# Performance work log

Measured on AMD Instinct MI355X. Metric: run time of the kernel, lower is better.

The kernel has to match this reference:

```python
import jax, jax.numpy as jnp
import numpy as np

N_E = 8192
DIM = 256
BETA = 0.25


def _l2norm(x, eps=1e-12):
    # matches F.normalize(p=2, dim=-1): x / max(||x||, eps)
    n = jnp.sqrt(jnp.sum(x * x, axis=-1, keepdims=True))
    return x / jnp.maximum(n, eps)


def setup_inputs() -> dict:
    key = jax.random.key(0)
    k1, k2 = jax.random.split(key)
    z = jax.random.normal(k1, (8, 1024, DIM), dtype=jnp.float32)
    embedding_weight = jax.random.normal(k2, (N_E, DIM), dtype=jnp.float32)
    return {"z": z, "embedding_weight": embedding_weight}


def reference(z, embedding_weight):
    z = _l2norm(z)                                   # [B,S,D]
    zf = z.reshape(-1, DIM)                          # [N,D]
    embed_norm = _l2norm(embedding_weight)           # [n_e,D]
    # d = ||z||^2 + ||e||^2 - 2 z.e  -> [N, n_e]
    d = (jnp.sum(zf * zf, axis=1, keepdims=True)
         + jnp.sum(embed_norm * embed_norm, axis=1)
         - 2.0 * jnp.einsum('bd,nd->bn', zf, embed_norm))
    encoding_indices = jnp.argmin(d, axis=1).reshape(z.shape[:-1])  # [B,S]
    z_q = embedding_weight[encoding_indices]          # gather raw codes
    z_q = _l2norm(z_q)                                # [B,S,D]
    loss = (BETA * jnp.mean((jax.lax.stop_gradient(z_q) - z) ** 2)
            + jnp.mean((z_q - jax.lax.stop_gradient(z)) ** 2))
    z_q = z + jax.lax.stop_gradient(z_q - z)          # straight-through
    return z_q, loss, encoding_indices
```

## Files before the change

kernel.cpp:

```cpp
#include <hip/hip_runtime.h>
#include <hip/hip_fp16.h>
#include <cfloat>
#include <math.h>

#define DIM    256
#define N_TOK  8192
#define N_E    8192
#define NSEG   1024
#define MARGIN 0.012f

typedef __attribute__((ext_vector_type(8))) short bf16x8;
typedef __attribute__((ext_vector_type(4))) float f32x4;
typedef __attribute__((ext_vector_type(8))) unsigned short ushort8;

__device__ __forceinline__ unsigned short f2bf(float f) {
    unsigned u = __float_as_uint(f);
    unsigned r = u + 0x7fff + ((u >> 16) & 1);
    return (unsigned short)(r >> 16);
}
__device__ __forceinline__ unsigned fkey(float f) {
    unsigned u = __float_as_uint(f);
    return (u & 0x80000000u) ? ~u : (u | 0x80000000u);
}
__device__ __forceinline__ unsigned short f2h(float f) {
    const __half h = __float2half(f);
    return *(const unsigned short*)&h;
}
__device__ __forceinline__ float h2f(unsigned short u) {
    __half_raw r; r.x = u;
    return __half2float((__half)r);
}

__global__ __launch_bounds__(256) void l2norm_all(const float* __restrict__ z,
                                                  const float* __restrict__ emb,
                                                  float* __restrict__ zn,
                                                  unsigned short* __restrict__ zb,
                                                  float* __restrict__ en,
                                                  unsigned short* __restrict__ esw,
                                                  float* __restrict__ e2) {
    const int lane = threadIdx.x & 63;
    const bool isE = blockIdx.x < (N_E / 4);
    const int row = (isE ? blockIdx.x : blockIdx.x - N_E / 4) * 4 + (threadIdx.x >> 6);
    const float* in = isE ? emb : z;
    float* out = isE ? en : zn;
    const float4 v = *(const float4*)(in + row * DIM + lane * 4);
    float s = v.x * v.x + v.y * v.y + v.z * v.z + v.w * v.w;
#pragma unroll
    for (int off = 1; off < 64; off <<= 1) s += __shfl_xor(s, off, 64);
    const float inv = 1.0f / fmaxf(sqrtf(s), 1e-12f);
    const float4 o = make_float4(v.x * inv, v.y * inv, v.z * inv, v.w * inv);
    *(float4*)(out + row * DIM + lane * 4) = o;
    ushort4 ob; ob.x = f2bf(o.x); ob.y = f2bf(o.y); ob.z = f2bf(o.z); ob.w = f2bf(o.w);
    const int k0 = lane * 4;
    if (isE) {
        const size_t sidx = ((size_t)((row >> 4) * 8 + (k0 >> 5)) * 64
                             + ((k0 >> 3) & 3) * 16 + (row & 15)) * 8 + (k0 & 7);
        *(ushort4*)(esw + sidx) = ob;
        float q = o.x * o.x + o.y * o.y + o.z * o.z + o.w * o.w;
#pragma unroll
        for (int off = 1; off < 64; off <<= 1) q += __shfl_xor(q, off, 64);
        if (lane == 0) e2[row] = q;
    } else {
        *(ushort4*)(zb + (size_t)row * DIM + k0) = ob;
    }
}

__global__ __launch_bounds__(256, 3) void mfma_dist(const unsigned short* __restrict__ zb,
                                                    const unsigned short* __restrict__ esw,
                                                    unsigned short* __restrict__ segMh) {
    __shared__ __align__(16) unsigned short As[2][128 * 64];
    float* sm = reinterpret_cast<float*>(As);

    const int tid  = threadIdx.x;
    const int lane = tid & 63;
    const int wave = tid >> 6;
    const int wm = wave & 1, wn = wave >> 1;
    const int row0 = (blockIdx.x & 63) * 128;
    const int col0 = (blockIdx.x >> 6) * 128;
    const int fr = lane & 15, q = lane >> 4;

    f32x4 acc[4][4];
#pragma unroll
    for (int ci = 0; ci < 4; ci++)
#pragma unroll
        for (int zi = 0; zi < 4; zi++) acc[ci][zi] = (f32x4){0.f, 0.f, 0.f, 0.f};

    const int aBase = (col0 >> 4) + wn * 4;
    auto la = [&](int i, int kc) {
        return *(const bf16x8*)(esw + (size_t)(aBase + i) * 4096 + kc * 512 + lane * 8);
    };
    const int cxor = (lane & 7) ^ ((lane >> 3) & 7);
    const unsigned short* gZ = zb + (size_t)(row0 + wave * 32 + (lane >> 3)) * DIM + cxor * 8;
    auto stage = [&](int buf, int p) {
#pragma unroll
        for (int j = 0; j < 4; j++) {
            __builtin_amdgcn_global_load_lds(
                (const __attribute__((address_space(1))) unsigned int*)(gZ + (size_t)j * 8 * DIM + p * 64),
                (__attribute__((address_space(3))) unsigned int*)&As[buf][(wave * 32 + j * 8) * 64],
                16, 0, 0);
        }
    };
    auto lz = [&](int buf, int i, int h) {
        const int r = wm * 64 + i * 16 + fr;
        const int slot = (h * 4 + q) ^ (fr & 7);
        return *(const bf16x8*)&As[buf][r * 64 + slot * 8];
    };

    bf16x8 ca[8][4];
    stage(0, 0);
    __builtin_amdgcn_sched_barrier(0);
#pragma unroll
    for (int kc = 0; kc < 2; kc++)
#pragma unroll
        for (int i = 0; i < 4; i++) ca[kc][i] = la(i, kc);

#pragma unroll
    for (int p = 0; p < 4; p++) {
        asm volatile("s_waitcnt vmcnt(8)" ::: "memory");
        __builtin_amdgcn_s_barrier();
        __builtin_amdgcn_sched_barrier(0);
        if (p < 3) {
            stage((p + 1) & 1, p + 1);
            __builtin_amdgcn_sched_barrier(0);
        }
#pragma unroll
        for (int h = 0; h < 2; h++) {
            const int kc = 2 * p + h;
            if (kc + 2 < 8) {
#pragma unroll
                for (int i = 0; i < 4; i++) ca[kc + 2][i] = la(i, kc + 2);
            }
            bf16x8 zfr[4];
#pragma unroll
            for (int i = 0; i < 4; i++) zfr[i] = lz(p & 1, i, h);
#pragma unroll
            for (int ci = 0; ci < 4; ci++)
#pragma unroll
                for (int zi = 0; zi < 4; zi++)
                    acc[ci][zi] = __builtin_amdgcn_mfma_f32_16x16x32_bf16(ca[kc][ci], zfr[zi], acc[ci][zi], 0, 0, 0);
        }
    }

#pragma unroll
    for (int ci = 0; ci < 4; ci++) {
#pragma unroll
        for (int zi = 0; zi < 4; zi++) {
            const float t0 = fmaf(-2.0f, acc[ci][zi][0], 1.0f);
            const float t1 = fmaf(-2.0f, acc[ci][zi][1], 1.0f);
            const float t2 = fmaf(-2.0f, acc[ci][zi][2], 1.0f);
            const float t3 = fmaf(-2.0f, acc[ci][zi][3], 1.0f);
            float mm = fminf(fminf(t0, t1), fminf(t2, t3));
            mm = fminf(mm, __shfl_xor(mm, 16, 64));
            if (q == 0) sm[wave * 512 + (ci * 2 + 0) * 64 + zi * 16 + fr] = mm;
            if (q == 2) sm[wave * 512 + (ci * 2 + 1) * 64 + zi * 16 + fr] = mm;
        }
    }
    ushort8 o8;
#pragma unroll
    for (int j = 0; j < 8; j++) o8[j] = f2h(sm[wave * 512 + j * 64 + lane]);
    *(ushort8*)&segMh[(size_t)(row0 + wm * 64 + lane) * NSEG + (col0 >> 3) + wn * 8] = o8;
}

__global__ __launch_bounds__(256) void select_rescore(const unsigned short* __restrict__ segMh,
                                                      const float* __restrict__ en,
                                                      const float* __restrict__ e2,
                                                      float* zq,
                                                      float* out_base,
                                                      float* __restrict__ pl) {
    const int lane = threadIdx.x & 63;
    const int row  = (blockIdx.x << 2) + (threadIdx.x >> 6);
    const unsigned short* ph = segMh + (size_t)row * NSEG + lane * 16;
    const ushort8 u0 = *(const ushort8*)ph;
    const ushort8 u1 = *(const ushort8*)(ph + 8);
    float vv[16];
#pragma unroll
    for (int j = 0; j < 8; j++) { vv[j] = h2f(u0[j]); vv[8 + j] = h2f(u1[j]); }
    float m = vv[0];
#pragma unroll
    for (int j = 1; j < 16; j++) m = fminf(m, vv[j]);
#pragma unroll
    for (int off = 1; off < 64; off <<= 1) m = fminf(m, __shfl_xor(m, off, 64));
    const float thr = m + MARGIN;

    const int q = lane >> 4, f = lane & 15;
    const float4* zp = (const float4*)(zq + (size_t)row * DIM);
    float4 z4[4];
#pragma unroll
    for (int j = 0; j < 4; j++) z4[j] = zp[j * 16 + f];

    unsigned long long pk = ~0ull;
#pragma unroll
    for (int j = 0; j < 16; j++) {
        unsigned long long bal = __ballot(vv[j] <= thr);
        while (bal) {
            const int l1 = __ffsll(bal) - 1; bal &= bal - 1;
            int l2 = l1;
            if (bal) { l2 = __ffsll(bal) - 1; bal &= bal - 1; }
            const int segA = l1 * 16 + j, segB = l2 * 16 + j;
            const int cA0 = segA * 8 + q,     cA1 = segA * 8 + 4 + q;
            const int cB0 = segB * 8 + q,     cB1 = segB * 8 + 4 + q;
            const float4* pA0 = (const float4*)(en + (size_t)cA0 * DIM);
            const float4* pA1 = (const float4*)(en + (size_t)cA1 * DIM);
            const float4* pB0 = (const float4*)(en + (size_t)cB0 * DIM);
            const float4* pB1 = (const float4*)(en + (size_t)cB1 * DIM);
            float4 eA0[4], eA1[4], eB0[4], eB1[4];
#pragma unroll
            for (int jj = 0; jj < 4; jj++) {
                eA0[jj] = pA0[jj * 16 + f]; eA1[jj] = pA1[jj * 16 + f];
                eB0[jj] = pB0[jj * 16 + f]; eB1[jj] = pB1[jj * 16 + f];
            }
            float sA0 = 0.f, sA1 = 0.f, sB0 = 0.f, sB1 = 0.f;
#pragma unroll
            for (int jj = 0; jj < 4; jj++) {
                sA0 = fmaf(z4[jj].x, eA0[jj].x, sA0); sA0 = fmaf(z4[jj].y, eA0[jj].y, sA0);
                sA0 = fmaf(z4[jj].z, eA0[jj].z, sA0); sA0 = fmaf(z4[jj].w, eA0[jj].w, sA0);
                sA1 = fmaf(z4[jj].x, eA1[jj].x, sA1); sA1 = fmaf(z4[jj].y, eA1[jj].y, sA1);
                sA1 = fmaf(z4[jj].z, eA1[jj].z, sA1); sA1 = fmaf(z4[jj].w, eA1[jj].w, sA1);
                sB0 = fmaf(z4[jj].x, eB0[jj].x, sB0); sB0 = fmaf(z4[jj].y, eB0[jj].y, sB0);
                sB0 = fmaf(z4[jj].z, eB0[jj].z, sB0); sB0 = fmaf(z4[jj].w, eB0[jj].w, sB0);
                sB1 = fmaf(z4[jj].x, eB1[jj].x, sB1); sB1 = fmaf(z4[jj].y, eB1[jj].y, sB1);
                sB1 = fmaf(z4[jj].z, eB1[jj].z, sB1); sB1 = fmaf(z4[jj].w, eB1[jj].w, sB1);
            }
#pragma unroll
            for (int off = 1; off < 16; off <<= 1) {
                sA0 += __shfl_xor(sA0, off, 64); sA1 += __shfl_xor(sA1, off, 64);
                sB0 += __shfl_xor(sB0, off, 64); sB1 += __shfl_xor(sB1, off, 64);
            }
            const float dA0 = fmaf(-2.0f, sA0, e2[cA0]);
            const float dA1 = fmaf(-2.0f, sA1, e2[cA1]);
            const float dB0 = fmaf(-2.0f, sB0, e2[cB0]);
            const float dB1 = fmaf(-2.0f, sB1, e2[cB1]);
            unsigned long long k;
            k = ((unsigned long long)fkey(dA0) << 32) | (unsigned)cA0; if (k < pk) pk = k;
            k = ((unsigned long long)fkey(dA1) << 32) | (unsigned)cA1; if (k < pk) pk = k;
            k = ((unsigned long long)fkey(dB0) << 32) | (unsigned)cB0; if (k < pk) pk = k;
            k = ((unsigned long long)fkey(dB1) << 32) | (unsigned)cB1; if (k < pk) pk = k;
        }
    }
#pragma unroll
    for (int off = 16; off < 64; off <<= 1) {
        const unsigned long long o = __shfl_xor(pk, off, 64);
        if (o < pk) pk = o;
    }
    const int i = (int)(pk & 0xffffffffu);

    const float4 qv = *(const float4*)(en + (size_t)i * DIM + lane * 4);
    const float4 zv = *(const float4*)(zq + (size_t)row * DIM + lane * 4);
    const float dx = qv.x - zv.x, dy = qv.y - zv.y, dz = qv.z - zv.z, dw = qv.w - zv.w;
    float s = dx * dx + dy * dy + dz * dz + dw * dw;
    *(float4*)(zq + (size_t)row * DIM + lane * 4) = qv;
#pragma unroll
    for (int off = 1; off < 64; off <<= 1) s += __shfl_xor(s, off, 64);
    if (lane == 0) {
        pl[row] = s;
        out_base[N_TOK * DIM + 1 + row] = (float)i;
    }
}

__global__ __launch_bounds__(1024) void finalize_loss(const float* __restrict__ pl,
                                                      float* __restrict__ out) {
    __shared__ float sw[16];
    const int t = threadIdx.x;
    float s = 0.f;
#pragma unroll
    for (int j = 0; j < 8; j++) s += pl[t + j * 1024];
#pragma unroll
    for (int off = 1; off < 64; off <<= 1) s += __shfl_xor(s, off, 64);
    if ((t & 63) == 0) sw[t >> 6] = s;
    __syncthreads();
    if (t < 16) {
        float v = sw[t];
#pragma unroll
        for (int off = 1; off < 16; off <<= 1) v += __shfl_xor(v, off, 64);
        if (t == 0) out[N_TOK * DIM] = v * (1.25f / 2097152.0f);
    }
}

extern "C" void kernel_launch(void* const* d_in, const int* in_sizes, int n_in,
                              void* d_out, int out_size, void* d_ws, size_t ws_size,
                              hipStream_t stream) {
    const float* z   = (const float*)d_in[0];
    const float* emb = (const float*)d_in[1];
    float* out = (float*)d_out;
    char* ws = (char*)d_ws;

    float*          en    = (float*)(ws);
    unsigned short* esw   = (unsigned short*)(ws + 8388608);
    unsigned short* zb    = (unsigned short*)(ws + 12582912);
    float*          e2    = (float*)(ws + 16777216);
    unsigned short* segMh = (unsigned short*)(ws + 16809984);
    float*          pl    = (float*)(ws + 33587200);

    l2norm_all<<<(N_E + N_TOK) / 4, 256, 0, stream>>>(z, emb, out, zb, en, esw, e2);
    mfma_dist<<<64 * 64, 256, 0, stream>>>(zb, esw, segMh);
    select_rescore<<<N_TOK / 4, 256, 0, stream>>>(segMh, en, e2, out, out, pl);
    finalize_loss<<<1, 1024, 0, stream>>>(pl, out);
}
```

Measured before the change: 137.4 us.

## Keep Z tile resident and sweep four codebook column tiles per block

Each block of the distance GEMM now loads its 128-row Z tile once (three chunks into LDS, the last two K-chunks straight into registers) and then loops over four 128-column codebook tiles. Codebook fragments are streamed from global memory through a rotating 8-slot register buffer. This cuts repeated Z staging and the grid shrinks from 4096 to 1024 blocks. In exchange the kernel uses more LDS and registers (launch bounds drop to 2 waves per SIMD) and has fewer blocks to hide latency.

```diff
diff --git a/kernel.cpp b/kernel.cpp
--- a/kernel.cpp
+++ b/kernel.cpp
@@ -65,100 +65,106 @@
     }
 }
 
-__global__ __launch_bounds__(256, 3) void mfma_dist(const unsigned short* __restrict__ zb,
+__global__ __launch_bounds__(256, 2) void mfma_dist(const unsigned short* __restrict__ zb,
                                                     const unsigned short* __restrict__ esw,
                                                     unsigned short* __restrict__ segMh) {
-    __shared__ __align__(16) unsigned short As[2][128 * 64];
-    float* sm = reinterpret_cast<float*>(As);
+    __shared__ __align__(16) unsigned short As[3][128 * 64];
+    __shared__ float smw[4][8][64];
 
     const int tid  = threadIdx.x;
     const int lane = tid & 63;
     const int wave = tid >> 6;
     const int wm = wave & 1, wn = wave >> 1;
-    const int row0 = (blockIdx.x & 63) * 128;
-    const int col0 = (blockIdx.x >> 6) * 128;
+    const int rb = blockIdx.x & 63;
+    const int cb = blockIdx.x >> 6;
+    const int row0 = rb * 128;
     const int fr = lane & 15, q = lane >> 4;
 
-    f32x4 acc[4][4];
-#pragma unroll
-    for (int ci = 0; ci < 4; ci++)
-#pragma unroll
-        for (int zi = 0; zi < 4; zi++) acc[ci][zi] = (f32x4){0.f, 0.f, 0.f, 0.f};
-
-    const int aBase = (col0 >> 4) + wn * 4;
-    auto la = [&](int i, int kc) {
-        return *(const bf16x8*)(esw + (size_t)(aBase + i) * 4096 + kc * 512 + lane * 8);
+    const unsigned short* ebase = esw + (size_t)(cb * 32 + wn * 4) * 4096 + lane * 8;
+    auto la = [&](int m, int i) {
+        return *(const bf16x8*)(ebase + (size_t)((m >> 3) * 8 + i) * 4096 + (m & 7) * 512);
     };
     const int cxor = (lane & 7) ^ ((lane >> 3) & 7);
     const unsigned short* gZ = zb + (size_t)(row0 + wave * 32 + (lane >> 3)) * DIM + cxor * 8;
-    auto stage = [&](int buf, int p) {
-#pragma unroll
-        for (int j = 0; j < 4; j++) {
+#pragma unroll
+    for (int p = 0; p < 3; p++)
+#pragma unroll
+        for (int j = 0; j < 4; j++)
             __builtin_amdgcn_global_load_lds(
                 (const __attribute__((address_space(1))) unsigned int*)(gZ + (size_t)j * 8 * DIM + p * 64),
-                (__attribute__((address_space(3))) unsigned int*)&As[buf][(wave * 32 + j * 8) * 64],
+                (__attribute__((address_space(3))) unsigned int*)&As[p][(wave * 32 + j * 8) * 64],
                 16, 0, 0);
-        }
+    __builtin_amdgcn_sched_barrier(0);
+    bf16x8 z67[2][4];
+#pragma unroll
+    for (int h = 0; h < 2; h++)
+#pragma unroll
+        for (int i = 0; i < 4; i++)
+            z67[h][i] = *(const bf16x8*)(zb + (size_t)(row0 + wm * 64 + i * 16 + fr) * DIM
+                                         + (6 + h) * 32 + q * 8);
+    __builtin_amdgcn_sched_barrier(0);
+    bf16x8 ca[8][4];
+#pragma unroll
+    for (int m = 0; m < 2; m++)
+#pragma unroll
+        for (int i = 0; i < 4; i++) ca[m][i] = la(m, i);
+    __builtin_amdgcn_sched_barrier(0);
+    asm volatile("s_waitcnt vmcnt(16)" ::: "memory");
+    __builtin_amdgcn_s_barrier();
+    __builtin_amdgcn_sched_barrier(0);
+
+    auto lz = [&](int kc, int i) {
+        const int r = wm * 64 + i * 16 + fr;
+        const int slot = ((kc & 1) * 4 + q) ^ (fr & 7);
+        return *(const bf16x8*)&As[kc >> 1][r * 64 + slot * 8];
     };
-    auto lz = [&](int buf, int i, int h) {
-        const int r = wm * 64 + i * 16 + fr;
-        const int slot = (h * 4 + q) ^ (fr & 7);
-        return *(const bf16x8*)&As[buf][r * 64 + slot * 8];
-    };
-
-    bf16x8 ca[8][4];
-    stage(0, 0);
-    __builtin_amdgcn_sched_barrier(0);
-#pragma unroll
-    for (int kc = 0; kc < 2; kc++)
-#pragma unroll
-        for (int i = 0; i < 4; i++) ca[kc][i] = la(i, kc);
-
-#pragma unroll
-    for (int p = 0; p < 4; p++) {
-        asm volatile("s_waitcnt vmcnt(8)" ::: "memory");
-        __builtin_amdgcn_s_barrier();
-        __builtin_amdgcn_sched_barrier(0);
-        if (p < 3) {
-            stage((p + 1) & 1, p + 1);
+
+#pragma unroll
+    for (int ct = 0; ct < 4; ct++) {
+        f32x4 acc[4][4];
+#pragma unroll
+        for (int ci = 0; ci < 4; ci++)
+#pragma unroll
+            for (int zi = 0; zi < 4; zi++) acc[ci][zi] = (f32x4){0.f, 0.f, 0.f, 0.f};
+
+#pragma unroll
+        for (int kc = 0; kc < 8; kc++) {
+            const int m = ct * 8 + kc;
+            if (m + 2 < 32) {
+#pragma unroll
+                for (int i = 0; i < 4; i++) ca[(m + 2) & 7][i] = la(m + 2, i);
+            }
+            bf16x8 zfr[4];
+#pragma unroll
+            for (int i = 0; i < 4; i++)
+                zfr[i] = (kc < 6) ? lz(kc, i) : z67[kc - 6][i];
+#pragma unroll
+            for (int ci = 0; ci < 4; ci++)
+#pragma unroll
+                for (int zi = 0; zi < 4; zi++)
+                    acc[ci][zi] = __builtin_amdgcn_mfma_f32_16x16x32_bf16(ca[kc][ci], zfr[zi], acc[ci][zi], 0, 0, 0);
             __builtin_amdgcn_sched_barrier(0);
         }
-#pragma unroll
-        for (int h = 0; h < 2; h++) {
-            const int kc = 2 * p + h;
-            if (kc + 2 < 8) {
-#pragma unroll
-                for (int i = 0; i < 4; i++) ca[kc + 2][i] = la(i, kc + 2);
-            }
-            bf16x8 zfr[4];
-#pragma unroll
-            for (int i = 0; i < 4; i++) zfr[i] = lz(p & 1, i, h);
-#pragma unroll
-            for (int ci = 0; ci < 4; ci++)
-#pragma unroll
-                for (int zi = 0; zi < 4; zi++)
-                    acc[ci][zi] = __builtin_amdgcn_mfma_f32_16x16x32_bf16(ca[kc][ci], zfr[zi], acc[ci][zi], 0, 0, 0);
+
+#pragma unroll
+        for (int ci = 0; ci < 4; ci++) {
+#pragma unroll
+            for (int zi = 0; zi < 4; zi++) {
+                const float t0 = fmaf(-2.0f, acc[ci][zi][0], 1.0f);
+                const float t1 = fmaf(-2.0f, acc[ci][zi][1], 1.0f);
+                const float t2 = fmaf(-2.0f, acc[ci][zi][2], 1.0f);
+                const float t3 = fmaf(-2.0f, acc[ci][zi][3], 1.0f);
+                float mm = fminf(fminf(t0, t1), fminf(t2, t3));
+                mm = fminf(mm, __shfl_xor(mm, 16, 64));
+                if (q == 0) smw[wave][ci * 2 + 0][zi * 16 + fr] = mm;
+                if (q == 2) smw[wave][ci * 2 + 1][zi * 16 + fr] = mm;
+            }
         }
-    }
-
-#pragma unroll
-    for (int ci = 0; ci < 4; ci++) {
-#pragma unroll
-        for (int zi = 0; zi < 4; zi++) {
-            const float t0 = fmaf(-2.0f, acc[ci][zi][0], 1.0f);
-            const float t1 = fmaf(-2.0f, acc[ci][zi][1], 1.0f);
-            const float t2 = fmaf(-2.0f, acc[ci][zi][2], 1.0f);
-            const float t3 = fmaf(-2.0f, acc[ci][zi][3], 1.0f);
-            float mm = fminf(fminf(t0, t1), fminf(t2, t3));
-            mm = fminf(mm, __shfl_xor(mm, 16, 64));
-            if (q == 0) sm[wave * 512 + (ci * 2 + 0) * 64 + zi * 16 + fr] = mm;
-            if (q == 2) sm[wave * 512 + (ci * 2 + 1) * 64 + zi * 16 + fr] = mm;
-        }
-    }
-    ushort8 o8;
-#pragma unroll
-    for (int j = 0; j < 8; j++) o8[j] = f2h(sm[wave * 512 + j * 64 + lane]);
-    *(ushort8*)&segMh[(size_t)(row0 + wm * 64 + lane) * NSEG + (col0 >> 3) + wn * 8] = o8;
+        ushort8 o8;
+#pragma unroll
+        for (int j = 0; j < 8; j++) o8[j] = f2h(smw[wave][j][lane]);
+        *(ushort8*)&segMh[(size_t)(row0 + wm * 64 + lane) * NSEG + cb * 64 + ct * 16 + wn * 8] = o8;
+    }
 }
 
 __global__ __launch_bounds__(256) void select_rescore(const unsigned short* __restrict__ segMh,
@@ -292,7 +298,7 @@
     float*          pl    = (float*)(ws + 33587200);
 
     l2norm_all<<<(N_E + N_TOK) / 4, 256, 0, stream>>>(z, emb, out, zb, en, esw, e2);
-    mfma_dist<<<64 * 64, 256, 0, stream>>>(zb, esw, segMh);
+    mfma_dist<<<1024, 256, 0, stream>>>(zb, esw, segMh);
     select_rescore<<<N_TOK / 4, 256, 0, stream>>>(segMh, en, e2, out, out, pl);
     finalize_loss<<<1, 1024, 0, stream>>>(pl, out);
 }
```

Result: faster. 128.8 us (median of 2 runs) (-6.2%).
